# Optimization experiments

Hardware: AMD Instinct MI355X
Metric: run time of the kernel (lower is better)

The kernel has to match this reference:

```python
import jax, jax.numpy as jnp
import numpy as np

MIN_E, MAX_E = 2, 10        # log2(min_window)=2, log2(max_window)=10
B, L = 64, 1 << 20          # batch, signal length (power of 2, >= max_window)
W_LEN = 2 * (1 << MAX_E) - 1  # 2*max_window - 1 = 2047


def setup_inputs() -> dict:
    key = jax.random.key(0)
    k1, k2, k3 = jax.random.split(key, 3)
    data = jax.random.normal(k1, (B, L), dtype=jnp.float32)
    stdev = 1.0 / np.sqrt(W_LEN).astype(np.float32)
    weights = jax.random.uniform(k2, (W_LEN,), dtype=jnp.float32, minval=-stdev, maxval=stdev)
    bias = jax.random.uniform(k3, (MAX_E,), dtype=jnp.float32, minval=-stdev, maxval=stdev)
    return {"data": data, "weights": weights, "bias": bias}


def reference(data, weights, bias):
    # Multi-scale time-scale convolution: for each scale s (window w = 2**s),
    # slide a w-tap filter (slice weights[w-1:2w-1], overlapping heap slices of
    # one shared weight vector) with stride w over the signal, add per-scale
    # bias, and write the k = L//w outputs into heap slots [k-1 : 2k-1] of a
    # flat output of length 2*L/min_window - 1.
    b, n = data.shape
    out_len = 2 * (n >> MIN_E) - 1
    out = jnp.zeros((b, out_len), dtype=data.dtype)
    for s in range(MIN_E, MAX_E + 1):
        w = 1 << s
        k = n // w
        taps = weights[w - 1 : 2 * w - 1]                       # [w]
        y = jnp.einsum('bkw,w->bk', data.reshape(b, k, w), taps)  # [b, k]
        y = y + bias[s - 1]
        out = out.at[:, k - 1 : 2 * k - 1].set(y)
    return out
```

## Files before the change

### kernel.cpp

```cpp
#include <hip/hip_runtime.h>

static constexpr int B_ = 64;
static constexpr int L_ = 1 << 20;
static constexpr int OUT_LEN = 2 * (L_ >> 2) - 1;

__device__ __forceinline__ float dot4(const float4& v, float t0, float t1, float t2, float t3) {
    return fmaf(v.x, t0, fmaf(v.y, t1, fmaf(v.z, t2, v.w * t3)));
}

template<int CTRL, int RM>
__device__ __forceinline__ float dpp_add(float v) {
    int t = __builtin_amdgcn_update_dpp(0, __builtin_bit_cast(int, v), CTRL, RM, 0xF, true);
    return v + __builtin_bit_cast(float, t);
}

template<int M>
__device__ __forceinline__ float seg_reduce(float v) {
    if constexpr (M >= 2)  v = dpp_add<0x111, 0xF>(v);
    if constexpr (M >= 4)  v = dpp_add<0x112, 0xF>(v);
    if constexpr (M >= 8)  v = dpp_add<0x114, 0xF>(v);
    if constexpr (M >= 16) v = dpp_add<0x118, 0xF>(v);
    if constexpr (M >= 32) v = dpp_add<0x142, 0xA>(v);
    if constexpr (M >= 64) v = dpp_add<0x143, 0xC>(v);
    return v;
}

template<int S>
__device__ __forceinline__ void scale_direct(const float4& v0, const float4& v1,
                                             const float4& v2, const float4& v3,
                                             const float* __restrict__ weights,
                                             const float* __restrict__ bias,
                                             float* __restrict__ orow, int c, int lane) {
    constexpr int w = 1 << S;
    constexpr int m = w >> 2;
    const float* tp = weights + (w - 1) + ((lane & (m - 1)) << 2);
    const float t0 = tp[0], t1 = tp[1], t2 = tp[2], t3 = tp[3];
    float p0 = seg_reduce<m>(dot4(v0, t0, t1, t2, t3));
    float p1 = seg_reduce<m>(dot4(v1, t0, t1, t2, t3));
    float p2 = seg_reduce<m>(dot4(v2, t0, t1, t2, t3));
    float p3 = seg_reduce<m>(dot4(v3, t0, t1, t2, t3));
    if ((lane & (m - 1)) == (m - 1)) {
        constexpr int base = (L_ >> S) - 1;
        constexpr int sps  = 256 >> S;
        const int seg = c * (1024 >> S) + (lane >> (S - 2));
        const float bs = bias[S - 1];
        orow[base + seg          ] = p0 + bs;
        orow[base + seg +     sps] = p1 + bs;
        orow[base + seg + 2 * sps] = p2 + bs;
        orow[base + seg + 3 * sps] = p3 + bs;
    }
}

template<int S>
__device__ __forceinline__ void scale_staged(const float4& v0, const float4& v1,
                                             const float4& v2, const float4& v3,
                                             const float* __restrict__ weights,
                                             const float* __restrict__ bias,
                                             float* __restrict__ lds, int ldsBase,
                                             int cc, int lane) {
    constexpr int w = 1 << S;
    constexpr int m = w >> 2;
    const float* tp = weights + (w - 1) + ((lane & (m - 1)) << 2);
    const float t0 = tp[0], t1 = tp[1], t2 = tp[2], t3 = tp[3];
    float p0 = seg_reduce<m>(dot4(v0, t0, t1, t2, t3));
    float p1 = seg_reduce<m>(dot4(v1, t0, t1, t2, t3));
    float p2 = seg_reduce<m>(dot4(v2, t0, t1, t2, t3));
    float p3 = seg_reduce<m>(dot4(v3, t0, t1, t2, t3));
    if ((lane & (m - 1)) == (m - 1)) {
        constexpr int per = 1024 >> S;
        constexpr int sps = 256 >> S;
        const int j = (lane >> (S - 2));
        const float bs = bias[S - 1];
        float* p = lds + ldsBase + cc * per + j;
        p[0      ] = p0 + bs;
        p[    sps] = p1 + bs;
        p[2 * sps] = p2 + bs;
        p[3 * sps] = p3 + bs;
    }
}

__global__ __launch_bounds__(1024) void multiscale_conv(
    const float* __restrict__ data,
    const float* __restrict__ weights,
    const float* __restrict__ bias,
    float* __restrict__ out)
{
    __shared__ float lds[1008];

    const int tid  = threadIdx.x;
    const int lane = tid & 63;
    const int cc   = tid >> 6;

    const int nblk = gridDim.x;
    const int bid  = blockIdx.x;
    const int sw   = (bid & 7) * (nblk >> 3) + (bid >> 3);

    const int g0 = sw * 16;
    const int g  = g0 + cc;
    const int b  = g >> 10;
    const int c  = g & 1023;
    const int c0 = g0 & 1023;

    const float4* dp = reinterpret_cast<const float4*>(data + (size_t)b * L_ + (size_t)c * 1024);
    const float4 v0 = dp[lane];
    const float4 v1 = dp[lane + 64];
    const float4 v2 = dp[lane + 128];
    const float4 v3 = dp[lane + 192];

    float* orow = out + (size_t)b * OUT_LEN;

    if (c0 == 0 && tid < 1023) orow[tid] = 0.0f;

    scale_direct<2>(v0, v1, v2, v3, weights, bias, orow, c, lane);
    scale_direct<3>(v0, v1, v2, v3, weights, bias, orow, c, lane);
    scale_direct<4>(v0, v1, v2, v3, weights, bias, orow, c, lane);

    scale_staged<5>(v0, v1, v2, v3, weights, bias, lds,   0, cc, lane);
    scale_staged<6>(v0, v1, v2, v3, weights, bias, lds, 512, cc, lane);
    scale_staged<7>(v0, v1, v2, v3, weights, bias, lds, 768, cc, lane);
    scale_staged<8>(v0, v1, v2, v3, weights, bias, lds, 896, cc, lane);

    {
        const float* ta = weights + 511 + (lane << 2);
        const float* tb = ta + 256;
        float p = dot4(v0, ta[0], ta[1], ta[2], ta[3]) + dot4(v1, tb[0], tb[1], tb[2], tb[3]);
        float q = dot4(v2, ta[0], ta[1], ta[2], ta[3]) + dot4(v3, tb[0], tb[1], tb[2], tb[3]);
        p = seg_reduce<64>(p);
        q = seg_reduce<64>(q);
        if (lane == 63) {
            const float bs = bias[8];
            lds[960 + 2 * cc    ] = p + bs;
            lds[960 + 2 * cc + 1] = q + bs;
        }
    }

    {
        const float* t = weights + 1023 + (lane << 2);
        float p = dot4(v0, t[0],   t[1],   t[2],   t[3]);
        p      += dot4(v1, t[256], t[257], t[258], t[259]);
        p      += dot4(v2, t[512], t[513], t[514], t[515]);
        p      += dot4(v3, t[768], t[769], t[770], t[771]);
        p = seg_reduce<64>(p);
        if (lane == 63) lds[992 + cc] = p + bias[9];
    }

    __syncthreads();

    if (tid < 1008) {
        const float v = lds[tid];
        size_t a;
        if      (tid < 512) a = (size_t)(32767) + (size_t)c0 * 32 + tid;
        else if (tid < 768) a = (size_t)(16383) + (size_t)c0 * 16 + (tid - 512);
        else if (tid < 896) a = (size_t)( 8191) + (size_t)c0 *  8 + (tid - 768);
        else if (tid < 960) a = (size_t)( 4095) + (size_t)c0 *  4 + (tid - 896);
        else if (tid < 992) a = (size_t)( 2047) + (size_t)c0 *  2 + (tid - 960);
        else                a = (size_t)( 1023) + (size_t)c0      + (tid - 992);
        orow[a] = v;
    }
}

extern "C" void kernel_launch(void* const* d_in, const int* in_sizes, int n_in,
                              void* d_out, int out_size, void* d_ws, size_t ws_size,
                              hipStream_t stream) {
    const float* data    = (const float*)d_in[0];
    const float* weights = (const float*)d_in[1];
    const float* bias    = (const float*)d_in[2];
    float* out = (float*)d_out;

    const int n_chunks = B_ * (L_ / 1024);
    dim3 grid(n_chunks / 16);
    dim3 block(1024);
    multiscale_conv<<<grid, block, 0, stream>>>(data, weights, bias, out);
}
```

Before: 91.71 us.

## Stage all scales through LDS and emit aligned float4 global stores

Fine scales 2-4 now also go through shared memory instead of scattered per-lane global writes. Each scale's region is written out with alignment-aware float4 stores plus scalar head and tail. Blocks shrink from 1024 to 256 threads (4 chunks per block, 4x more blocks), and the zeroing of the unused prefix is vectorised. The goal is fewer, wider store transactions and better occupancy, at the cost of more LDS traffic and extra index arithmetic.

```diff
diff --git a/kernel.cpp b/kernel.cpp
--- a/kernel.cpp
+++ b/kernel.cpp
@@ -25,39 +25,14 @@
     return v;
 }
 
-template<int S>
-__device__ __forceinline__ void scale_direct(const float4& v0, const float4& v1,
-                                             const float4& v2, const float4& v3,
-                                             const float* __restrict__ weights,
-                                             const float* __restrict__ bias,
-                                             float* __restrict__ orow, int c, int lane) {
-    constexpr int w = 1 << S;
-    constexpr int m = w >> 2;
-    const float* tp = weights + (w - 1) + ((lane & (m - 1)) << 2);
-    const float t0 = tp[0], t1 = tp[1], t2 = tp[2], t3 = tp[3];
-    float p0 = seg_reduce<m>(dot4(v0, t0, t1, t2, t3));
-    float p1 = seg_reduce<m>(dot4(v1, t0, t1, t2, t3));
-    float p2 = seg_reduce<m>(dot4(v2, t0, t1, t2, t3));
-    float p3 = seg_reduce<m>(dot4(v3, t0, t1, t2, t3));
-    if ((lane & (m - 1)) == (m - 1)) {
-        constexpr int base = (L_ >> S) - 1;
-        constexpr int sps  = 256 >> S;
-        const int seg = c * (1024 >> S) + (lane >> (S - 2));
-        const float bs = bias[S - 1];
-        orow[base + seg          ] = p0 + bs;
-        orow[base + seg +     sps] = p1 + bs;
-        orow[base + seg + 2 * sps] = p2 + bs;
-        orow[base + seg + 3 * sps] = p3 + bs;
-    }
-}
+__host__ __device__ constexpr int lds_base(int S) { return S == 2 ? 0 : 2048 - (8192 >> S); }
 
 template<int S>
-__device__ __forceinline__ void scale_staged(const float4& v0, const float4& v1,
-                                             const float4& v2, const float4& v3,
-                                             const float* __restrict__ weights,
-                                             const float* __restrict__ bias,
-                                             float* __restrict__ lds, int ldsBase,
-                                             int cc, int lane) {
+__device__ __forceinline__ void scale_stage(const float4& v0, const float4& v1,
+                                            const float4& v2, const float4& v3,
+                                            const float* __restrict__ weights,
+                                            const float* __restrict__ bias,
+                                            float* __restrict__ lds, int cc, int lane) {
     constexpr int w = 1 << S;
     constexpr int m = w >> 2;
     const float* tp = weights + (w - 1) + ((lane & (m - 1)) << 2);
@@ -69,9 +44,9 @@
     if ((lane & (m - 1)) == (m - 1)) {
         constexpr int per = 1024 >> S;
         constexpr int sps = 256 >> S;
-        const int j = (lane >> (S - 2));
+        const int j = lane >> (S - 2);
         const float bs = bias[S - 1];
-        float* p = lds + ldsBase + cc * per + j;
+        float* p = lds + lds_base(S) + cc * per + j;
         p[0      ] = p0 + bs;
         p[    sps] = p1 + bs;
         p[2 * sps] = p2 + bs;
@@ -79,13 +54,32 @@
     }
 }
 
-__global__ __launch_bounds__(1024) void multiscale_conv(
+template<int S>
+__device__ __forceinline__ void write_region(float* __restrict__ out, size_t rowbase, int c0,
+                                             const float* __restrict__ lds, int t) {
+    constexpr int N  = 4096 >> S;
+    constexpr int LB = lds_base(S);
+    const size_t A = rowbase + (size_t)((L_ >> S) - 1) + (size_t)c0 * (1024 >> S);
+    float* gp = out + A;
+    const int h = (int)((4 - (A & 3)) & 3);
+    const int K = (N - h) >> 2;
+    const int r = N - h - 4 * K;
+    if (t < K) {
+        const int i = h + 4 * t;
+        float4 v = make_float4(lds[LB + i], lds[LB + i + 1], lds[LB + i + 2], lds[LB + i + 3]);
+        *reinterpret_cast<float4*>(gp + i) = v;
+    }
+    if (t < h) gp[t] = lds[LB + t];
+    if (t < r) gp[N - r + t] = lds[LB + N - r + t];
+}
+
+__global__ __launch_bounds__(256) void multiscale_conv(
     const float* __restrict__ data,
     const float* __restrict__ weights,
     const float* __restrict__ bias,
     float* __restrict__ out)
 {
-    __shared__ float lds[1008];
+    __shared__ float lds[2044];
 
     const int tid  = threadIdx.x;
     const int lane = tid & 63;
@@ -95,30 +89,26 @@
     const int bid  = blockIdx.x;
     const int sw   = (bid & 7) * (nblk >> 3) + (bid >> 3);
 
-    const int g0 = sw * 16;
+    const int g0 = sw * 4;
     const int g  = g0 + cc;
     const int b  = g >> 10;
-    const int c  = g & 1023;
     const int c0 = g0 & 1023;
 
-    const float4* dp = reinterpret_cast<const float4*>(data + (size_t)b * L_ + (size_t)c * 1024);
+    const float4* dp = reinterpret_cast<const float4*>(data + (size_t)b * L_ + (size_t)(g & 1023) * 1024);
     const float4 v0 = dp[lane];
     const float4 v1 = dp[lane + 64];
     const float4 v2 = dp[lane + 128];
     const float4 v3 = dp[lane + 192];
 
-    float* orow = out + (size_t)b * OUT_LEN;
+    const size_t rowbase = (size_t)b * OUT_LEN;
 
-    if (c0 == 0 && tid < 1023) orow[tid] = 0.0f;
-
-    scale_direct<2>(v0, v1, v2, v3, weights, bias, orow, c, lane);
-    scale_direct<3>(v0, v1, v2, v3, weights, bias, orow, c, lane);
-    scale_direct<4>(v0, v1, v2, v3, weights, bias, orow, c, lane);
-
-    scale_staged<5>(v0, v1, v2, v3, weights, bias, lds,   0, cc, lane);
-    scale_staged<6>(v0, v1, v2, v3, weights, bias, lds, 512, cc, lane);
-    scale_staged<7>(v0, v1, v2, v3, weights, bias, lds, 768, cc, lane);
-    scale_staged<8>(v0, v1, v2, v3, weights, bias, lds, 896, cc, lane);
+    scale_stage<2>(v0, v1, v2, v3, weights, bias, lds, cc, lane);
+    scale_stage<3>(v0, v1, v2, v3, weights, bias, lds, cc, lane);
+    scale_stage<4>(v0, v1, v2, v3, weights, bias, lds, cc, lane);
+    scale_stage<5>(v0, v1, v2, v3, weights, bias, lds, cc, lane);
+    scale_stage<6>(v0, v1, v2, v3, weights, bias, lds, cc, lane);
+    scale_stage<7>(v0, v1, v2, v3, weights, bias, lds, cc, lane);
+    scale_stage<8>(v0, v1, v2, v3, weights, bias, lds, cc, lane);
 
     {
         const float* ta = weights + 511 + (lane << 2);
@@ -129,8 +119,8 @@
         q = seg_reduce<64>(q);
         if (lane == 63) {
             const float bs = bias[8];
-            lds[960 + 2 * cc    ] = p + bs;
-            lds[960 + 2 * cc + 1] = q + bs;
+            lds[2032 + 2 * cc    ] = p + bs;
+            lds[2032 + 2 * cc + 1] = q + bs;
         }
     }
 
@@ -141,21 +131,29 @@
         p      += dot4(v2, t[512], t[513], t[514], t[515]);
         p      += dot4(v3, t[768], t[769], t[770], t[771]);
         p = seg_reduce<64>(p);
-        if (lane == 63) lds[992 + cc] = p + bias[9];
+        if (lane == 63) lds[2040 + cc] = p + bias[9];
     }
 
     __syncthreads();
 
-    if (tid < 1008) {
-        const float v = lds[tid];
-        size_t a;
-        if      (tid < 512) a = (size_t)(32767) + (size_t)c0 * 32 + tid;
-        else if (tid < 768) a = (size_t)(16383) + (size_t)c0 * 16 + (tid - 512);
-        else if (tid < 896) a = (size_t)( 8191) + (size_t)c0 *  8 + (tid - 768);
-        else if (tid < 960) a = (size_t)( 4095) + (size_t)c0 *  4 + (tid - 896);
-        else if (tid < 992) a = (size_t)( 2047) + (size_t)c0 *  2 + (tid - 960);
-        else                a = (size_t)( 1023) + (size_t)c0      + (tid - 992);
-        orow[a] = v;
+    write_region<2>(out, rowbase, c0, lds, tid);
+    write_region<3>(out, rowbase, c0, lds, tid);
+    write_region<4>(out, rowbase, c0, lds, tid);
+    write_region<5>(out, rowbase, c0, lds, tid);
+    write_region<6>(out, rowbase, c0, lds, tid);
+    write_region<7>(out, rowbase, c0, lds, tid);
+    write_region<8>(out, rowbase, c0, lds, tid);
+    if (tid < 8) out[rowbase + 2047 + (size_t)c0 * 2 + tid] = lds[2032 + tid];
+    if (tid < 4) out[rowbase + 1023 + (size_t)c0     + tid] = lds[2040 + tid];
+
+    if (c0 == 0) {
+        float* gp = out + rowbase;
+        const int h = (int)((4 - (rowbase & 3)) & 3);
+        const int K = (1023 - h) >> 2;
+        const int r = 1023 - h - 4 * K;
+        if (tid < h) gp[tid] = 0.0f;
+        if (tid < K) *reinterpret_cast<float4*>(gp + h + 4 * tid) = make_float4(0.f, 0.f, 0.f, 0.f);
+        if (tid < r) gp[1023 - r + tid] = 0.0f;
     }
 }
 
@@ -168,7 +166,7 @@
     float* out = (float*)d_out;
 
     const int n_chunks = B_ * (L_ / 1024);
-    dim3 grid(n_chunks / 16);
-    dim3 block(1024);
+    dim3 grid(n_chunks / 4);
+    dim3 block(256);
     multiscale_conv<<<grid, block, 0, stream>>>(data, weights, bias, out);
 }
```

Result: faster. 86.08 us (-6.1%).
